# Kernel tuning notes

Measured on AMD Instinct MI355X. Metric: run time of the kernel, lower is better.

Reference implementation:

```python
import jax, jax.numpy as jnp
import numpy as np
import math

N_HEAD = 16


def _alibi_slopes(n_head):
    def get_slopes(n):
        start = 2.0 ** (-2.0 ** (-(math.log2(n) - 3)))
        return [start * start ** i for i in range(n)]
    if math.log2(n_head).is_integer():
        slopes = get_slopes(n_head)
    else:
        c = 2 ** math.floor(math.log2(n_head))
        slopes = get_slopes(c)
        extra = get_slopes(2 * c)[0::2]
        slopes = slopes + extra[: n_head - c]
    return np.asarray(slopes, dtype=np.float32)


def setup_inputs() -> dict:
    key = jax.random.key(0)
    ks = jax.random.split(key, 9)
    B, S, E = 2, 2048, 1024
    sd = 1.0 / math.sqrt(E)
    inp = {
        "x": jax.random.normal(ks[0], (B, S, E), jnp.float32),
        "Wq": jax.random.uniform(ks[1], (E, E), jnp.float32, -sd, sd),
        "bq": jnp.zeros((E,), jnp.float32),
        "Wk": jax.random.uniform(ks[2], (E, E), jnp.float32, -sd, sd),
        "bk": jnp.zeros((E,), jnp.float32),
        "Wv": jax.random.uniform(ks[3], (E, E), jnp.float32, -sd, sd),
        "bv": jnp.zeros((E,), jnp.float32),
        "Wo": jax.random.uniform(ks[4], (E, E), jnp.float32, -sd, sd),
        "bo": jnp.zeros((E,), jnp.float32),
        "alibi_slopes": jnp.asarray(_alibi_slopes(N_HEAD)),
    }
    return inp


def reference(x, Wq, bq, Wk, bk, Wv, bv, Wo, bo, alibi_slopes):
    B, S, E = x.shape
    H = N_HEAD
    hd = E // H
    scale = hd ** -0.5
    # Linear layers (torch Linear: y = x @ W.T + b)
    Q = (x @ Wq.T + bq).reshape(B, H, S, hd)  # faithful: view, NOT transpose
    K = (x @ Wk.T + bk).reshape(B, H, S, hd)
    V = (x @ Wv.T + bv).reshape(B, H, S, hd)
    scores = jnp.einsum("bhqd,bhkd->bhqk", Q, K) * scale
    pos = jnp.arange(S)
    rel = jnp.abs(pos[None, :] - pos[:, None]).astype(scores.dtype)  # [S,S]
    bias = alibi_slopes[None, :, None, None] * rel[None, None]  # [1,H,S,S]
    scores = scores - bias
    probs = jax.nn.softmax(scores, axis=-1)
    # faithful quirk: keep only head index 1's probs, broadcast to all heads
    probs1 = probs[:, 1:2, :, :]  # [B,1,S,S]
    attn_out = jnp.matmul(probs1, V)  # broadcast -> [B,H,S,hd]
    attn_out = attn_out.reshape(B, S, E)
    out = attn_out @ Wo.T + bo
    return (out, probs1)
```

## Files before the change

kernel.cpp:

```cpp
#include <hip/hip_runtime.h>

typedef __bf16 bf16;
typedef __bf16 bf16_4 __attribute__((ext_vector_type(4)));
typedef __bf16 bf16_8 __attribute__((ext_vector_type(8)));
typedef float f32_4 __attribute__((ext_vector_type(4)));

#define GLDS16(g, l) \
  __builtin_amdgcn_global_load_lds((const __attribute__((address_space(1))) unsigned int*)(g), \
                                   (__attribute__((address_space(3))) unsigned int*)(l), 16, 0, 0)

__global__ __launch_bounds__(256) void convert_all(
    const float* __restrict__ x, const float* __restrict__ wq, const float* __restrict__ wk,
    const float* __restrict__ wv, const float* __restrict__ wo,
    bf16* __restrict__ xb, bf16* __restrict__ wqb, bf16* __restrict__ wkb,
    bf16* __restrict__ wvb, bf16* __restrict__ wob)
{
    int i = blockIdx.x * 256 + threadIdx.x;
    const float* s; bf16* d; int off;
    if (i < 1048576) { s = x; d = xb; off = i; }
    else {
        int j = i - 1048576;
        int sel = j >> 18;
        off = j & 262143;
        s = (sel == 0) ? wq : (sel == 1) ? wk : (sel == 2) ? wv : wo;
        d = (sel == 0) ? wqb : (sel == 1) ? wkb : (sel == 2) ? wvb : wob;
    }
    float4 v = reinterpret_cast<const float4*>(s)[off];
    bf16_4 o; o.x = (bf16)v.x; o.y = (bf16)v.y; o.z = (bf16)v.z; o.w = (bf16)v.w;
    reinterpret_cast<bf16_4*>(d)[off] = o;
}

template<int BM, int MODE>
__global__ __launch_bounds__(256) void gemm_glds(
    const bf16* __restrict__ A, int lda, long long aBatch,
    const bf16* __restrict__ W, int ldw, long long wBatch,
    const float* __restrict__ bias,
    void* __restrict__ outp, long long outBatch,
    int N, int K, float scale, const float* __restrict__ slopes,
    const bf16* __restrict__ W2, const float* __restrict__ bias2, void* __restrict__ out2,
    const bf16* __restrict__ W3, const float* __restrict__ bias3, void* __restrict__ out3,
    float* __restrict__ spart, const float* __restrict__ rsinv)
{
    constexpr int CA = BM * 8;
    constexpr int NJ = (BM == 128) ? 4 : 2;
    __shared__ alignas(16) bf16 As[BM * 64];
    __shared__ alignas(16) bf16 Bs[128 * 64];

    const int tid  = threadIdx.x;
    const int lane = tid & 63;
    const int wave = tid >> 6;
    const int l15  = lane & 15;
    const int quad = lane >> 4;
    const int n0   = blockIdx.x * 128;
    const int z    = blockIdx.z;

    const int WM = (BM == 128) ? (wave >> 1) * 64 : 0;
    const int WN = (BM == 128) ? (wave & 1) * 64 : wave * 32;

    int m0;
    const bf16* Ab; const bf16* Wb; const float* bvec; void* op;
    long long obase;
    if (MODE == 11) {
        int y = blockIdx.y;
        if (y < 64) {
            m0 = y * 64;
            Ab = A; Wb = W; bvec = bias; op = outp; obase = 0;
        } else {
            int sub   = y - 64;
            int batch = (sub >> 1) & 1;
            int sel   = sub >> 2;
            m0   = (sub & 1) * 64;
            Ab   = A + (long long)batch * 2097152LL + 131072LL;
            Wb   = sel ? W3 : W2;
            bvec = sel ? bias3 : bias2;
            op   = sel ? out3 : out2;
            obase = (long long)batch * 131072LL;
        }
    } else {
        m0 = blockIdx.y * BM;
        Ab = A + (long long)z * aBatch; Wb = W + (long long)z * wBatch;
        bvec = bias; op = outp;
        obase = (long long)z * outBatch;
    }

    f32_4 acc[4][NJ];
#pragma unroll
    for (int i = 0; i < 4; i++)
#pragma unroll
        for (int j = 0; j < NJ; j++) acc[i][j] = (f32_4)(0.0f);

    for (int k0 = 0; k0 < K; k0 += 64) {
#pragma unroll
        for (int it = 0; it < CA / 256; ++it) {
            int p = wave * (CA / 4) + it * 64 + lane;
            int r = p >> 3;
            int q = (p & 7) ^ (r & 7);
            GLDS16(Ab + (long long)(m0 + r) * lda + k0 + q * 8, As + p * 8);
        }
#pragma unroll
        for (int it = 0; it < 4; ++it) {
            int p = wave * 256 + it * 64 + lane;
            int r = p >> 3;
            int q = (p & 7) ^ (r & 7);
            GLDS16(Wb + (long long)(n0 + r) * ldw + k0 + q * 8, Bs + p * 8);
        }
        __syncthreads();

#pragma unroll
        for (int kh = 0; kh < 2; ++kh) {
            bf16_8 af[4], bfr[NJ];
#pragma unroll
            for (int t = 0; t < 4; ++t) {
                int r = WM + t * 16 + l15;
                int q = (kh * 4 + quad) ^ (r & 7);
                af[t] = *reinterpret_cast<const bf16_8*>(&As[r * 64 + q * 8]);
            }
#pragma unroll
            for (int j = 0; j < NJ; ++j) {
                int r = WN + j * 16 + l15;
                int q = (kh * 4 + quad) ^ (r & 7);
                bfr[j] = *reinterpret_cast<const bf16_8*>(&Bs[r * 64 + q * 8]);
            }
#pragma unroll
            for (int i = 0; i < 4; ++i)
#pragma unroll
                for (int j = 0; j < NJ; ++j)
                    acc[i][j] = __builtin_amdgcn_mfma_f32_16x16x32_bf16(af[i], bfr[j], acc[i][j], 0, 0, 0);
        }
        __syncthreads();
    }

    if constexpr (MODE == 9) {
        const float slope = slopes[1];
#pragma unroll
        for (int i = 0; i < 4; i++) {
#pragma unroll
            for (int rg = 0; rg < 4; rg++) {
                int m = m0 + WM + i * 16 + quad * 4 + rg;
                float rowpart = 0.0f;
#pragma unroll
                for (int j = 0; j < NJ; j++) {
                    int n = n0 + WN + j * 16 + l15;
                    float v = acc[i][j][rg] * scale - slope * fabsf((float)(m - n));
                    float e = __expf(v);
                    rowpart += e;
                    ((bf16*)op)[obase + (long long)m * N + n] = (bf16)e;
                }
                rowpart += __shfl_xor(rowpart, 1, 64);
                rowpart += __shfl_xor(rowpart, 2, 64);
                rowpart += __shfl_xor(rowpart, 4, 64);
                rowpart += __shfl_xor(rowpart, 8, 64);
                if (l15 == 0)
                    spart[((long long)z * 2048 + m) * 32 + (n0 >> 6) + (WN >> 6)] = rowpart;
            }
        }
        return;
    }

#pragma unroll
    for (int i = 0; i < 4; i++) {
#pragma unroll
        for (int j = 0; j < NJ; j++) {
#pragma unroll
            for (int rg = 0; rg < 4; rg++) {
                int m = m0 + WM + i * 16 + quad * 4 + rg;
                int n = n0 + WN + j * 16 + l15;
                float v = acc[i][j][rg];
                if (MODE == 11) {
                    v += bvec[n];
                    ((bf16*)op)[obase + (long long)m * 1024 + n] = (bf16)v;
                } else if (MODE == 1) {
                    if (bvec) v += bvec[n];
                    ((float*)op)[obase + (long long)m * N + n] = v;
                } else {
                    v *= rsinv[(long long)z * 2048 + m];
                    long long off = obase +
                                    ((long long)(n >> 6)) * 131072LL + (long long)m * 64 + (n & 63);
                    ((bf16*)op)[off] = (bf16)v;
                }
            }
        }
    }
}

__global__ __launch_bounds__(256) void transpose_v(const unsigned short* __restrict__ v,
                                                   unsigned short* __restrict__ vt) {
    __shared__ unsigned short tile[64 * 66];
    const int t  = threadIdx.x;
    const int k0 = blockIdx.x * 64;
    const int h  = blockIdx.y;
    const int b  = blockIdx.z;
    const unsigned short* src = v + (long long)b * 2097152LL + (long long)h * 131072LL;
#pragma unroll
    for (int p = 0; p < 8; p++) {
        int idx = t + p * 256;
        int k   = idx >> 5;
        int dc  = idx & 31;
        ushort2 u = *reinterpret_cast<const ushort2*>(&src[(long long)(k0 + k) * 64 + dc * 2]);
        tile[(dc * 2) * 66 + k]     = u.x;
        tile[(dc * 2 + 1) * 66 + k] = u.y;
    }
    __syncthreads();
    unsigned short* dst = vt + (long long)b * 2097152LL + (long long)h * 64 * 2048LL + k0;
#pragma unroll
    for (int p = 0; p < 8; p++) {
        int idx = t + p * 256;
        int d   = idx >> 5;
        int kc  = idx & 31;
        ushort2 u;
        u.x = tile[d * 66 + kc * 2];
        u.y = tile[d * 66 + kc * 2 + 1];
        *reinterpret_cast<ushort2*>(&dst[(long long)d * 2048 + kc * 2]) = u;
    }
}

__global__ __launch_bounds__(256) void normalize_rows(const float* __restrict__ spart,
                                                      const bf16* __restrict__ pb,
                                                      float* __restrict__ probs_f,
                                                      float* __restrict__ rsinv) {
    __shared__ float inv_s;
    const long long row = blockIdx.x;
    const int t = threadIdx.x;

    if (t < 64) {
        float p = (t < 32) ? spart[row * 32 + t] : 0.0f;
#pragma unroll
        for (int o = 1; o <= 32; o <<= 1) p += __shfl_xor(p, o, 64);
        if (t == 0) { float inv = 1.0f / p; inv_s = inv; rsinv[row] = inv; }
    }
    __syncthreads();
    const float inv = inv_s;

    bf16_8 e = reinterpret_cast<const bf16_8*>(pb + row * 2048LL)[t];
    float4 o0, o1;
    o0.x = (float)e[0] * inv; o0.y = (float)e[1] * inv; o0.z = (float)e[2] * inv; o0.w = (float)e[3] * inv;
    o1.x = (float)e[4] * inv; o1.y = (float)e[5] * inv; o1.z = (float)e[6] * inv; o1.w = (float)e[7] * inv;
    reinterpret_cast<float4*>(probs_f + row * 2048LL)[t * 2]     = o0;
    reinterpret_cast<float4*>(probs_f + row * 2048LL)[t * 2 + 1] = o1;
}

extern "C" void kernel_launch(void* const* d_in, const int* in_sizes, int n_in,
                              void* d_out, int out_size, void* d_ws, size_t ws_size,
                              hipStream_t stream) {
    const float* x      = (const float*)d_in[0];
    const float* Wq     = (const float*)d_in[1];
    const float* bq     = (const float*)d_in[2];
    const float* Wk     = (const float*)d_in[3];
    const float* bk     = (const float*)d_in[4];
    const float* Wv     = (const float*)d_in[5];
    const float* bv     = (const float*)d_in[6];
    const float* Wo     = (const float*)d_in[7];
    const float* bo     = (const float*)d_in[8];
    const float* slopes = (const float*)d_in[9];

    char* w = (char*)d_ws;
    bf16* x_bf  = (bf16*)w;  w += 4096LL * 1024 * 2;
    bf16* wq_bf = (bf16*)w;  w += 1024LL * 1024 * 2;
    bf16* wk_bf = (bf16*)w;  w += 1024LL * 1024 * 2;
    bf16* wv_bf = (bf16*)w;  w += 1024LL * 1024 * 2;
    bf16* wo_bf = (bf16*)w;  w += 1024LL * 1024 * 2;
    bf16* qh1   = (bf16*)w;  w += 2LL * 131072 * 2;
    bf16* kh1   = (bf16*)w;  w += 2LL * 131072 * 2;
    bf16* v_bf  = (bf16*)w;  w += 4096LL * 1024 * 2;
    bf16* vt    = (bf16*)w;  w += 2LL * 1024 * 2048 * 2;
    bf16* attn  = (bf16*)w;  w += 4096LL * 1024 * 2;
    bf16* pb    = (bf16*)w;  w += 2LL * 2048 * 2048 * 2;
    float* spart = (float*)w; w += 4096LL * 32 * 4;
    float* rsinv = (float*)w; w += 4096LL * 4;

    float* out_f   = (float*)d_out;
    float* probs_f = (float*)d_out + 4194304LL;

    convert_all<<<8192, 256, 0, stream>>>(x, Wq, Wk, Wv, Wo, x_bf, wq_bf, wk_bf, wv_bf, wo_bf);

    gemm_glds<64, 11><<<dim3(8, 72, 1), 256, 0, stream>>>(
        x_bf, 1024, 0LL,
        wv_bf, 1024, 0LL, bv, v_bf, 0LL, 1024, 1024, 1.0f, nullptr,
        wq_bf, bq, qh1,
        wk_bf, bk, kh1,
        nullptr, nullptr);

    transpose_v<<<dim3(32, 16, 2), 256, 0, stream>>>((const unsigned short*)v_bf,
                                                     (unsigned short*)vt);

    gemm_glds<128, 9><<<dim3(16, 16, 2), 256, 0, stream>>>(
        qh1, 64, 131072LL, kh1, 64, 131072LL, nullptr,
        pb, 4194304LL, 2048, 64, 0.125f, slopes,
        nullptr, nullptr, nullptr, nullptr, nullptr, nullptr, spart, nullptr);

    normalize_rows<<<4096, 256, 0, stream>>>(spart, pb, probs_f, rsinv);

    gemm_glds<64, 6><<<dim3(8, 32, 2), 256, 0, stream>>>(
        pb, 2048, 4194304LL, vt, 2048, 2097152LL, nullptr,
        attn, 2097152LL, 1024, 2048, 1.0f, nullptr,
        nullptr, nullptr, nullptr, nullptr, nullptr, nullptr, nullptr, rsinv);

    gemm_glds<64, 1><<<dim3(8, 64, 1), 256, 0, stream>>>(
        attn, 1024, 0LL, wo_bf, 1024, 0LL, bo,
        out_f, 0LL, 1024, 1024, 1.0f, nullptr,
        nullptr, nullptr, nullptr, nullptr, nullptr, nullptr, nullptr, nullptr);
}
```

Before: 195.5 us.

## Fuse all attention stages into one cooperative persistent kernel with grid syncs

Replaces the seven separate launches (convert, QKV GEMM, V transpose, scores, normalize, PV GEMM, output GEMM) with one cooperative kernel of 512 blocks that runs each stage in turn, separated by grid-wide syncs. The aim is to remove per-launch overhead and the idle gaps between kernels. The cost is that each stage is now fixed to 512 blocks, so phases such as the Q/K projection leave most blocks idle, and every grid sync adds a barrier. If the cooperative launch fails, the code falls back to the original multi-kernel path.

```diff
diff --git a/kernel.cpp b/kernel.cpp
--- a/kernel.cpp
+++ b/kernel.cpp
@@ -1,4 +1,7 @@
 #include <hip/hip_runtime.h>
+#include <hip/hip_cooperative_groups.h>
+
+namespace cg = cooperative_groups;
 
 typedef __bf16 bf16;
 typedef __bf16 bf16_4 __attribute__((ext_vector_type(4)));
@@ -8,6 +11,282 @@
 #define GLDS16(g, l) \
   __builtin_amdgcn_global_load_lds((const __attribute__((address_space(1))) unsigned int*)(g), \
                                    (__attribute__((address_space(3))) unsigned int*)(l), 16, 0, 0)
+
+template<int BM>
+__device__ __forceinline__ void gemm_core(
+    const bf16* __restrict__ Ab, int lda,
+    const bf16* __restrict__ Wb, int ldw,
+    int K, int m0, int n0, int tid,
+    bf16* As, bf16* Bs,
+    f32_4 (&acc)[4][(BM == 128) ? 4 : 2])
+{
+    constexpr int NJ = (BM == 128) ? 4 : 2;
+    constexpr int CA = BM * 8;
+    const int lane = tid & 63;
+    const int wave = tid >> 6;
+    const int l15  = lane & 15;
+    const int quad = lane >> 4;
+    const int WM = (BM == 128) ? (wave >> 1) * 64 : 0;
+    const int WN = (BM == 128) ? (wave & 1) * 64 : wave * 32;
+
+#pragma unroll
+    for (int i = 0; i < 4; i++)
+#pragma unroll
+        for (int j = 0; j < NJ; j++) acc[i][j] = (f32_4)(0.0f);
+
+    for (int k0 = 0; k0 < K; k0 += 64) {
+#pragma unroll
+        for (int it = 0; it < CA / 256; ++it) {
+            int p = wave * (CA / 4) + it * 64 + lane;
+            int r = p >> 3;
+            int q = (p & 7) ^ (r & 7);
+            GLDS16(Ab + (long long)(m0 + r) * lda + k0 + q * 8, As + p * 8);
+        }
+#pragma unroll
+        for (int it = 0; it < 4; ++it) {
+            int p = wave * 256 + it * 64 + lane;
+            int r = p >> 3;
+            int q = (p & 7) ^ (r & 7);
+            GLDS16(Wb + (long long)(n0 + r) * ldw + k0 + q * 8, Bs + p * 8);
+        }
+        __syncthreads();
+
+#pragma unroll
+        for (int kh = 0; kh < 2; ++kh) {
+            bf16_8 af[4], bfr[NJ];
+#pragma unroll
+            for (int t = 0; t < 4; ++t) {
+                int r = WM + t * 16 + l15;
+                int q = (kh * 4 + quad) ^ (r & 7);
+                af[t] = *reinterpret_cast<const bf16_8*>(&As[r * 64 + q * 8]);
+            }
+#pragma unroll
+            for (int j = 0; j < NJ; ++j) {
+                int r = WN + j * 16 + l15;
+                int q = (kh * 4 + quad) ^ (r & 7);
+                bfr[j] = *reinterpret_cast<const bf16_8*>(&Bs[r * 64 + q * 8]);
+            }
+#pragma unroll
+            for (int i = 0; i < 4; ++i)
+#pragma unroll
+                for (int j = 0; j < NJ; ++j)
+                    acc[i][j] = __builtin_amdgcn_mfma_f32_16x16x32_bf16(af[i], bfr[j], acc[i][j], 0, 0, 0);
+        }
+        __syncthreads();
+    }
+}
+
+__global__ __launch_bounds__(256, 2) void fused_mha(
+    const float* __restrict__ x,  const float* __restrict__ Wq, const float* __restrict__ bq,
+    const float* __restrict__ Wk, const float* __restrict__ bk,
+    const float* __restrict__ Wv, const float* __restrict__ bv,
+    const float* __restrict__ Wo, const float* __restrict__ bo,
+    const float* __restrict__ slopes,
+    bf16* __restrict__ x_bf, bf16* __restrict__ wq_bf, bf16* __restrict__ wk_bf,
+    bf16* __restrict__ wv_bf, bf16* __restrict__ wo_bf,
+    bf16* __restrict__ qh1, bf16* __restrict__ kh1, bf16* __restrict__ v_bf,
+    bf16* __restrict__ vt, bf16* __restrict__ attn, bf16* __restrict__ pb,
+    float* __restrict__ spart, float* __restrict__ rsinv,
+    float* __restrict__ out_f, float* __restrict__ probs_f)
+{
+    cg::grid_group grid = cg::this_grid();
+    __shared__ alignas(16) char smem[32768];
+    bf16* As    = (bf16*)smem;
+    bf16* Bs64  = (bf16*)(smem + 8192);
+    bf16* Bs128 = (bf16*)(smem + 16384);
+    const int tid = threadIdx.x;
+    const int bid = blockIdx.x;
+    const int lane = tid & 63;
+    const int wave = tid >> 6;
+    const int l15  = lane & 15;
+    const int quad = lane >> 4;
+
+    for (int i = bid * 256 + tid; i < 2097152; i += 512 * 256) {
+        const float* s; bf16* d; int off;
+        if (i < 1048576) { s = x; d = x_bf; off = i; }
+        else {
+            int j = i - 1048576;
+            int sel = j >> 18;
+            off = j & 262143;
+            s = (sel == 0) ? Wq : (sel == 1) ? Wk : (sel == 2) ? Wv : Wo;
+            d = (sel == 0) ? wq_bf : (sel == 1) ? wk_bf : (sel == 2) ? wv_bf : wo_bf;
+        }
+        float4 v = reinterpret_cast<const float4*>(s)[off];
+        bf16_4 o; o.x = (bf16)v.x; o.y = (bf16)v.y; o.z = (bf16)v.z; o.w = (bf16)v.w;
+        reinterpret_cast<bf16_4*>(d)[off] = o;
+    }
+    grid.sync();
+
+    {
+        int m0 = (bid >> 3) * 64, n0 = (bid & 7) * 128;
+        f32_4 acc[4][2];
+        gemm_core<64>(x_bf, 1024, wv_bf, 1024, 1024, m0, n0, tid, As, Bs64, acc);
+        const int WN = wave * 32;
+#pragma unroll
+        for (int i = 0; i < 4; i++)
+#pragma unroll
+            for (int j = 0; j < 2; j++)
+#pragma unroll
+                for (int rg = 0; rg < 4; rg++) {
+                    int m = m0 + i * 16 + quad * 4 + rg;
+                    int n = n0 + WN + j * 16 + l15;
+                    v_bf[(long long)m * 1024 + n] = (bf16)(acc[i][j][rg] + bv[n]);
+                }
+    }
+    grid.sync();
+
+    if (bid < 64) {
+        int sub = bid >> 3, xx = bid & 7;
+        int batch = (sub >> 1) & 1, sel = sub >> 2;
+        int m0 = (sub & 1) * 64, n0 = xx * 128;
+        const bf16* Ab = x_bf + (long long)batch * 2097152LL + 131072LL;
+        const bf16* Wb = sel ? wk_bf : wq_bf;
+        const float* bvec = sel ? bk : bq;
+        bf16* op = sel ? kh1 : qh1;
+        long long obase = (long long)batch * 131072LL;
+        f32_4 acc[4][2];
+        gemm_core<64>(Ab, 1024, Wb, 1024, 1024, m0, n0, tid, As, Bs64, acc);
+        const int WN = wave * 32;
+#pragma unroll
+        for (int i = 0; i < 4; i++)
+#pragma unroll
+            for (int j = 0; j < 2; j++)
+#pragma unroll
+                for (int rg = 0; rg < 4; rg++) {
+                    int m = m0 + i * 16 + quad * 4 + rg;
+                    int n = n0 + WN + j * 16 + l15;
+                    op[obase + (long long)m * 1024 + n] = (bf16)(acc[i][j][rg] + bvec[n]);
+                }
+    } else {
+        unsigned short* tile = (unsigned short*)smem;
+        const unsigned short* vsrc = (const unsigned short*)v_bf;
+        unsigned short* vdst = (unsigned short*)vt;
+        for (int u = bid - 64; u < 1024; u += 448) {
+            int k0 = (u & 31) * 64, h = (u >> 5) & 15, b = u >> 9;
+            const unsigned short* src = vsrc + (long long)b * 2097152LL + (long long)h * 131072LL;
+#pragma unroll
+            for (int p = 0; p < 8; p++) {
+                int idx = tid + p * 256;
+                int k = idx >> 5, dc = idx & 31;
+                ushort2 uu = *reinterpret_cast<const ushort2*>(&src[(long long)(k0 + k) * 64 + dc * 2]);
+                tile[(dc * 2) * 66 + k]     = uu.x;
+                tile[(dc * 2 + 1) * 66 + k] = uu.y;
+            }
+            __syncthreads();
+            unsigned short* dst = vdst + (long long)b * 2097152LL + (long long)h * 64 * 2048LL + k0;
+#pragma unroll
+            for (int p = 0; p < 8; p++) {
+                int idx = tid + p * 256;
+                int d = idx >> 5, kc = idx & 31;
+                ushort2 uu;
+                uu.x = tile[d * 66 + kc * 2];
+                uu.y = tile[d * 66 + kc * 2 + 1];
+                *reinterpret_cast<ushort2*>(&dst[(long long)d * 2048 + kc * 2]) = uu;
+            }
+            __syncthreads();
+        }
+    }
+    grid.sync();
+
+    {
+        int z = bid >> 8, rem = bid & 255;
+        int m0 = (rem >> 4) * 128, n0 = (rem & 15) * 128;
+        const bf16* Ab = qh1 + (long long)z * 131072LL;
+        const bf16* Wb = kh1 + (long long)z * 131072LL;
+        f32_4 acc[4][4];
+        gemm_core<128>(Ab, 64, Wb, 64, 64, m0, n0, tid, As, Bs128, acc);
+        const int WM = (wave >> 1) * 64;
+        const int WN = (wave & 1) * 64;
+        const float slope = slopes[1];
+        long long obase = (long long)z * 4194304LL;
+#pragma unroll
+        for (int i = 0; i < 4; i++) {
+#pragma unroll
+            for (int rg = 0; rg < 4; rg++) {
+                int m = m0 + WM + i * 16 + quad * 4 + rg;
+                float rowpart = 0.0f;
+#pragma unroll
+                for (int j = 0; j < 4; j++) {
+                    int n = n0 + WN + j * 16 + l15;
+                    float v = acc[i][j][rg] * 0.125f - slope * fabsf((float)(m - n));
+                    float e = __expf(v);
+                    rowpart += e;
+                    pb[obase + (long long)m * 2048 + n] = (bf16)e;
+                }
+                rowpart += __shfl_xor(rowpart, 1, 64);
+                rowpart += __shfl_xor(rowpart, 2, 64);
+                rowpart += __shfl_xor(rowpart, 4, 64);
+                rowpart += __shfl_xor(rowpart, 8, 64);
+                if (l15 == 0)
+                    spart[((long long)z * 2048 + m) * 32 + (n0 >> 6) + (WN >> 6)] = rowpart;
+            }
+        }
+    }
+    grid.sync();
+
+    {
+        float* invp = (float*)smem;
+        for (int r = bid; r < 4096; r += 512) {
+            if (tid < 64) {
+                float p = (tid < 32) ? spart[(long long)r * 32 + tid] : 0.0f;
+#pragma unroll
+                for (int o = 1; o <= 32; o <<= 1) p += __shfl_xor(p, o, 64);
+                if (tid == 0) { float inv = 1.0f / p; invp[0] = inv; rsinv[r] = inv; }
+            }
+            __syncthreads();
+            float inv = invp[0];
+            bf16_8 e = reinterpret_cast<const bf16_8*>(pb + (long long)r * 2048)[tid];
+            float4 o0, o1;
+            o0.x = (float)e[0] * inv; o0.y = (float)e[1] * inv; o0.z = (float)e[2] * inv; o0.w = (float)e[3] * inv;
+            o1.x = (float)e[4] * inv; o1.y = (float)e[5] * inv; o1.z = (float)e[6] * inv; o1.w = (float)e[7] * inv;
+            reinterpret_cast<float4*>(probs_f + (long long)r * 2048)[tid * 2]     = o0;
+            reinterpret_cast<float4*>(probs_f + (long long)r * 2048)[tid * 2 + 1] = o1;
+            __syncthreads();
+        }
+    }
+    grid.sync();
+
+    {
+        int z = bid >> 8, rem = bid & 255;
+        int m0 = (rem >> 3) * 64, n0 = (rem & 7) * 128;
+        const bf16* Ab = pb + (long long)z * 4194304LL;
+        const bf16* Wb = vt + (long long)z * 2097152LL;
+        f32_4 acc[4][2];
+        gemm_core<64>(Ab, 2048, Wb, 2048, 2048, m0, n0, tid, As, Bs64, acc);
+        const int WN = wave * 32;
+        long long obase = (long long)z * 2097152LL;
+#pragma unroll
+        for (int i = 0; i < 4; i++)
+#pragma unroll
+            for (int j = 0; j < 2; j++)
+#pragma unroll
+                for (int rg = 0; rg < 4; rg++) {
+                    int m = m0 + i * 16 + quad * 4 + rg;
+                    int n = n0 + WN + j * 16 + l15;
+                    float v = acc[i][j][rg] * rsinv[(long long)z * 2048 + m];
+                    long long off = obase + ((long long)(n >> 6)) * 131072LL + (long long)m * 64 + (n & 63);
+                    attn[off] = (bf16)v;
+                }
+    }
+    grid.sync();
+
+    {
+        int m0 = (bid >> 3) * 64, n0 = (bid & 7) * 128;
+        f32_4 acc[4][2];
+        gemm_core<64>(attn, 1024, wo_bf, 1024, 1024, m0, n0, tid, As, Bs64, acc);
+        const int WN = wave * 32;
+#pragma unroll
+        for (int i = 0; i < 4; i++)
+#pragma unroll
+            for (int j = 0; j < 2; j++)
+#pragma unroll
+                for (int rg = 0; rg < 4; rg++) {
+                    int m = m0 + i * 16 + quad * 4 + rg;
+                    int n = n0 + WN + j * 16 + l15;
+                    out_f[(long long)m * 1024 + n] = acc[i][j][rg] + bo[n];
+                }
+    }
+}
 
 __global__ __launch_bounds__(256) void convert_all(
     const float* __restrict__ x, const float* __restrict__ wq, const float* __restrict__ wk,
@@ -41,19 +320,16 @@
     const bf16* __restrict__ W3, const float* __restrict__ bias3, void* __restrict__ out3,
     float* __restrict__ spart, const float* __restrict__ rsinv)
 {
-    constexpr int CA = BM * 8;
     constexpr int NJ = (BM == 128) ? 4 : 2;
     __shared__ alignas(16) bf16 As[BM * 64];
     __shared__ alignas(16) bf16 Bs[128 * 64];
-
-    const int tid  = threadIdx.x;
+    const int tid = threadIdx.x;
     const int lane = tid & 63;
     const int wave = tid >> 6;
-    const int l15  = lane & 15;
+    const int l15 = lane & 15;
     const int quad = lane >> 4;
-    const int n0   = blockIdx.x * 128;
-    const int z    = blockIdx.z;
-
+    const int n0 = blockIdx.x * 128;
+    const int z = blockIdx.z;
     const int WM = (BM == 128) ? (wave >> 1) * 64 : 0;
     const int WN = (BM == 128) ? (wave & 1) * 64 : wave * 32;
 
@@ -62,25 +338,20 @@
     long long obase;
     if (MODE == 11) {
         int y = blockIdx.y;
-        if (y < 64) {
-            m0 = y * 64;
-            Ab = A; Wb = W; bvec = bias; op = outp; obase = 0;
-        } else {
-            int sub   = y - 64;
+        if (y < 64) { m0 = y * 64; Ab = A; Wb = W; bvec = bias; op = outp; obase = 0; }
+        else {
+            int sub = y - 64;
             int batch = (sub >> 1) & 1;
-            int sel   = sub >> 2;
-            m0   = (sub & 1) * 64;
-            Ab   = A + (long long)batch * 2097152LL + 131072LL;
-            Wb   = sel ? W3 : W2;
-            bvec = sel ? bias3 : bias2;
-            op   = sel ? out3 : out2;
+            int sel = sub >> 2;
+            m0 = (sub & 1) * 64;
+            Ab = A + (long long)batch * 2097152LL + 131072LL;
+            Wb = sel ? W3 : W2; bvec = sel ? bias3 : bias2; op = sel ? out3 : out2;
             obase = (long long)batch * 131072LL;
         }
     } else {
         m0 = blockIdx.y * BM;
         Ab = A + (long long)z * aBatch; Wb = W + (long long)z * wBatch;
-        bvec = bias; op = outp;
-        obase = (long long)z * outBatch;
+        bvec = bias; op = outp; obase = (long long)z * outBatch;
     }
 
     f32_4 acc[4][NJ];
@@ -91,8 +362,8 @@
 
     for (int k0 = 0; k0 < K; k0 += 64) {
 #pragma unroll
-        for (int it = 0; it < CA / 256; ++it) {
-            int p = wave * (CA / 4) + it * 64 + lane;
+        for (int it = 0; it < (BM * 8) / 256; ++it) {
+            int p = wave * (BM * 2) + it * 64 + lane;
             int r = p >> 3;
             int q = (p & 7) ^ (r & 7);
             GLDS16(Ab + (long long)(m0 + r) * lda + k0 + q * 8, As + p * 8);
@@ -105,7 +376,6 @@
             GLDS16(Wb + (long long)(n0 + r) * ldw + k0 + q * 8, Bs + p * 8);
         }
         __syncthreads();
-
 #pragma unroll
         for (int kh = 0; kh < 2; ++kh) {
             bf16_8 af[4], bfr[NJ];
@@ -174,8 +444,7 @@
                     ((float*)op)[obase + (long long)m * N + n] = v;
                 } else {
                     v *= rsinv[(long long)z * 2048 + m];
-                    long long off = obase +
-                                    ((long long)(n >> 6)) * 131072LL + (long long)m * 64 + (n & 63);
+                    long long off = obase + ((long long)(n >> 6)) * 131072LL + (long long)m * 64 + (n & 63);
                     ((bf16*)op)[off] = (bf16)v;
                 }
             }
@@ -186,18 +455,17 @@
 __global__ __launch_bounds__(256) void transpose_v(const unsigned short* __restrict__ v,
                                                    unsigned short* __restrict__ vt) {
     __shared__ unsigned short tile[64 * 66];
-    const int t  = threadIdx.x;
+    const int t = threadIdx.x;
     const int k0 = blockIdx.x * 64;
-    const int h  = blockIdx.y;
-    const int b  = blockIdx.z;
+    const int h = blockIdx.y;
+    const int b = blockIdx.z;
     const unsigned short* src = v + (long long)b * 2097152LL + (long long)h * 131072LL;
 #pragma unroll
     for (int p = 0; p < 8; p++) {
         int idx = t + p * 256;
-        int k   = idx >> 5;
-        int dc  = idx & 31;
+        int k = idx >> 5, dc = idx & 31;
         ushort2 u = *reinterpret_cast<const ushort2*>(&src[(long long)(k0 + k) * 64 + dc * 2]);
-        tile[(dc * 2) * 66 + k]     = u.x;
+        tile[(dc * 2) * 66 + k] = u.x;
         tile[(dc * 2 + 1) * 66 + k] = u.y;
     }
     __syncthreads();
@@ -205,8 +473,7 @@
 #pragma unroll
     for (int p = 0; p < 8; p++) {
         int idx = t + p * 256;
-        int d   = idx >> 5;
-        int kc  = idx & 31;
+        int d = idx >> 5, kc = idx & 31;
         ushort2 u;
         u.x = tile[d * 66 + kc * 2];
         u.y = tile[d * 66 + kc * 2 + 1];
@@ -221,7 +488,6 @@
     __shared__ float inv_s;
     const long long row = blockIdx.x;
     const int t = threadIdx.x;
-
     if (t < 64) {
         float p = (t < 32) ? spart[row * 32 + t] : 0.0f;
 #pragma unroll
@@ -230,12 +496,11 @@
     }
     __syncthreads();
     const float inv = inv_s;
-
     bf16_8 e = reinterpret_cast<const bf16_8*>(pb + row * 2048LL)[t];
     float4 o0, o1;
     o0.x = (float)e[0] * inv; o0.y = (float)e[1] * inv; o0.z = (float)e[2] * inv; o0.w = (float)e[3] * inv;
     o1.x = (float)e[4] * inv; o1.y = (float)e[5] * inv; o1.z = (float)e[6] * inv; o1.w = (float)e[7] * inv;
-    reinterpret_cast<float4*>(probs_f + row * 2048LL)[t * 2]     = o0;
+    reinterpret_cast<float4*>(probs_f + row * 2048LL)[t * 2] = o0;
     reinterpret_cast<float4*>(probs_f + row * 2048LL)[t * 2 + 1] = o1;
 }
 
@@ -271,32 +536,34 @@
     float* out_f   = (float*)d_out;
     float* probs_f = (float*)d_out + 4194304LL;
 
-    convert_all<<<8192, 256, 0, stream>>>(x, Wq, Wk, Wv, Wo, x_bf, wq_bf, wk_bf, wv_bf, wo_bf);
-
-    gemm_glds<64, 11><<<dim3(8, 72, 1), 256, 0, stream>>>(
-        x_bf, 1024, 0LL,
-        wv_bf, 1024, 0LL, bv, v_bf, 0LL, 1024, 1024, 1.0f, nullptr,
-        wq_bf, bq, qh1,
-        wk_bf, bk, kh1,
-        nullptr, nullptr);
-
-    transpose_v<<<dim3(32, 16, 2), 256, 0, stream>>>((const unsigned short*)v_bf,
-                                                     (unsigned short*)vt);
-
-    gemm_glds<128, 9><<<dim3(16, 16, 2), 256, 0, stream>>>(
-        qh1, 64, 131072LL, kh1, 64, 131072LL, nullptr,
-        pb, 4194304LL, 2048, 64, 0.125f, slopes,
-        nullptr, nullptr, nullptr, nullptr, nullptr, nullptr, spart, nullptr);
-
-    normalize_rows<<<4096, 256, 0, stream>>>(spart, pb, probs_f, rsinv);
-
-    gemm_glds<64, 6><<<dim3(8, 32, 2), 256, 0, stream>>>(
-        pb, 2048, 4194304LL, vt, 2048, 2097152LL, nullptr,
-        attn, 2097152LL, 1024, 2048, 1.0f, nullptr,
-        nullptr, nullptr, nullptr, nullptr, nullptr, nullptr, nullptr, rsinv);
-
-    gemm_glds<64, 1><<<dim3(8, 64, 1), 256, 0, stream>>>(
-        attn, 1024, 0LL, wo_bf, 1024, 0LL, bo,
-        out_f, 0LL, 1024, 1024, 1.0f, nullptr,
-        nullptr, nullptr, nullptr, nullptr, nullptr, nullptr, nullptr, nullptr);
-}
+    void* args[] = {
+        (void*)&x, (void*)&Wq, (void*)&bq, (void*)&Wk, (void*)&bk,
+        (void*)&Wv, (void*)&bv, (void*)&Wo, (void*)&bo, (void*)&slopes,
+        (void*)&x_bf, (void*)&wq_bf, (void*)&wk_bf, (void*)&wv_bf, (void*)&wo_bf,
+        (void*)&qh1, (void*)&kh1, (void*)&v_bf, (void*)&vt, (void*)&attn, (void*)&pb,
+        (void*)&spart, (void*)&rsinv, (void*)&out_f, (void*)&probs_f
+    };
+    hipError_t err = hipLaunchCooperativeKernel((void*)fused_mha, dim3(512), dim3(256),
+                                                args, 0, stream);
+    if (err != hipSuccess) {
+        convert_all<<<8192, 256, 0, stream>>>(x, Wq, Wk, Wv, Wo, x_bf, wq_bf, wk_bf, wv_bf, wo_bf);
+        gemm_glds<64, 11><<<dim3(8, 72, 1), 256, 0, stream>>>(
+            x_bf, 1024, 0LL, wv_bf, 1024, 0LL, bv, v_bf, 0LL, 1024, 1024, 1.0f, nullptr,
+            wq_bf, bq, qh1, wk_bf, bk, kh1, nullptr, nullptr);
+        transpose_v<<<dim3(32, 16, 2), 256, 0, stream>>>((const unsigned short*)v_bf,
+                                                         (unsigned short*)vt);
+        gemm_glds<128, 9><<<dim3(16, 16, 2), 256, 0, stream>>>(
+            qh1, 64, 131072LL, kh1, 64, 131072LL, nullptr,
+            pb, 4194304LL, 2048, 64, 0.125f, slopes,
+            nullptr, nullptr, nullptr, nullptr, nullptr, nullptr, spart, nullptr);
+        normalize_rows<<<4096, 256, 0, stream>>>(spart, pb, probs_f, rsinv);
+        gemm_glds<64, 6><<<dim3(8, 32, 2), 256, 0, stream>>>(
+            pb, 2048, 4194304LL, vt, 2048, 2097152LL, nullptr,
+            attn, 2097152LL, 1024, 2048, 1.0f, nullptr,
+            nullptr, nullptr, nullptr, nullptr, nullptr, nullptr, nullptr, rsinv);
+        gemm_glds<64, 1><<<dim3(8, 64, 1), 256, 0, stream>>>(
+            attn, 1024, 0LL, wo_bf, 1024, 0LL, bo,
+            out_f, 0LL, 1024, 1024, 1.0f, nullptr,
+            nullptr, nullptr, nullptr, nullptr, nullptr, nullptr, nullptr, nullptr);
+    }
+}
```

Result: slower. 568.2 us (+190.7%).

## Fuse V transpose into scores kernel and row normalization into PV GEMM

Applied to the files above, without the earlier changes.

Folds the separate V-transpose launch into the tail of the scores kernel, where each block transposes two 64x64 tiles after writing its exp scores. The normalize_rows kernel is removed: the PV GEMM now sums the per-row partial sums itself and writes the fp32 normalized probabilities from the P tiles already staged in LDS, one diagonal k-chunk per column block. This drops two launches and a second full read of the bf16 exp matrix, in exchange for extra work and barriers inside the scores and PV kernels. The generic templated GEMM is also split into specialised kernels.

```diff
diff --git a/kernel.cpp b/kernel.cpp
--- a/kernel.cpp
+++ b/kernel.cpp
@@ -30,60 +30,23 @@
     reinterpret_cast<bf16_4*>(d)[off] = o;
 }
 
-template<int BM, int MODE>
-__global__ __launch_bounds__(256) void gemm_glds(
-    const bf16* __restrict__ A, int lda, long long aBatch,
-    const bf16* __restrict__ W, int ldw, long long wBatch,
-    const float* __restrict__ bias,
-    void* __restrict__ outp, long long outBatch,
-    int N, int K, float scale, const float* __restrict__ slopes,
-    const bf16* __restrict__ W2, const float* __restrict__ bias2, void* __restrict__ out2,
-    const bf16* __restrict__ W3, const float* __restrict__ bias3, void* __restrict__ out3,
-    float* __restrict__ spart, const float* __restrict__ rsinv)
-{
+template<int BM>
+__device__ __forceinline__ void gemm_core(
+    const bf16* __restrict__ Ab, int lda,
+    const bf16* __restrict__ Wb, int ldw,
+    int K, int m0, int n0, int tid,
+    bf16* As, bf16* Bs,
+    f32_4 (&acc)[4][(BM == 128) ? 4 : 2])
+{
+    constexpr int NJ = (BM == 128) ? 4 : 2;
     constexpr int CA = BM * 8;
-    constexpr int NJ = (BM == 128) ? 4 : 2;
-    __shared__ alignas(16) bf16 As[BM * 64];
-    __shared__ alignas(16) bf16 Bs[128 * 64];
-
-    const int tid  = threadIdx.x;
     const int lane = tid & 63;
     const int wave = tid >> 6;
     const int l15  = lane & 15;
     const int quad = lane >> 4;
-    const int n0   = blockIdx.x * 128;
-    const int z    = blockIdx.z;
-
     const int WM = (BM == 128) ? (wave >> 1) * 64 : 0;
     const int WN = (BM == 128) ? (wave & 1) * 64 : wave * 32;
 
-    int m0;
-    const bf16* Ab; const bf16* Wb; const float* bvec; void* op;
-    long long obase;
-    if (MODE == 11) {
-        int y = blockIdx.y;
-        if (y < 64) {
-            m0 = y * 64;
-            Ab = A; Wb = W; bvec = bias; op = outp; obase = 0;
-        } else {
-            int sub   = y - 64;
-            int batch = (sub >> 1) & 1;
-            int sel   = sub >> 2;
-            m0   = (sub & 1) * 64;
-            Ab   = A + (long long)batch * 2097152LL + 131072LL;
-            Wb   = sel ? W3 : W2;
-            bvec = sel ? bias3 : bias2;
-            op   = sel ? out3 : out2;
-            obase = (long long)batch * 131072LL;
-        }
-    } else {
-        m0 = blockIdx.y * BM;
-        Ab = A + (long long)z * aBatch; Wb = W + (long long)z * wBatch;
-        bvec = bias; op = outp;
-        obase = (long long)z * outBatch;
-    }
-
-    f32_4 acc[4][NJ];
 #pragma unroll
     for (int i = 0; i < 4; i++)
 #pragma unroll
@@ -129,114 +92,265 @@
         }
         __syncthreads();
     }
-
-    if constexpr (MODE == 9) {
-        const float slope = slopes[1];
-#pragma unroll
-        for (int i = 0; i < 4; i++) {
+}
+
+__global__ __launch_bounds__(256) void proj_merged(
+    const bf16* __restrict__ x_bf,
+    const bf16* __restrict__ wv_bf, const float* __restrict__ bv, bf16* __restrict__ v_bf,
+    const bf16* __restrict__ wq_bf, const float* __restrict__ bq, bf16* __restrict__ qh1,
+    const bf16* __restrict__ wk_bf, const float* __restrict__ bk, bf16* __restrict__ kh1)
+{
+    __shared__ alignas(16) bf16 As[64 * 64];
+    __shared__ alignas(16) bf16 Bs[128 * 64];
+    const int tid = threadIdx.x;
+    const int lane = tid & 63, wave = tid >> 6, l15 = lane & 15, quad = lane >> 4;
+    const int n0 = blockIdx.x * 128;
+
+    int m0;
+    const bf16* Ab; const bf16* Wb; const float* bvec; bf16* op;
+    long long obase;
+    int y = blockIdx.y;
+    if (y < 64) { m0 = y * 64; Ab = x_bf; Wb = wv_bf; bvec = bv; op = v_bf; obase = 0; }
+    else {
+        int sub = y - 64;
+        int batch = (sub >> 1) & 1;
+        int sel = sub >> 2;
+        m0 = (sub & 1) * 64;
+        Ab = x_bf + (long long)batch * 2097152LL + 131072LL;
+        Wb = sel ? wk_bf : wq_bf;
+        bvec = sel ? bk : bq;
+        op = sel ? kh1 : qh1;
+        obase = (long long)batch * 131072LL;
+    }
+
+    f32_4 acc[4][2];
+    gemm_core<64>(Ab, 1024, Wb, 1024, 1024, m0, n0, tid, As, Bs, acc);
+
+    const int WN = wave * 32;
+#pragma unroll
+    for (int i = 0; i < 4; i++)
+#pragma unroll
+        for (int j = 0; j < 2; j++)
 #pragma unroll
             for (int rg = 0; rg < 4; rg++) {
-                int m = m0 + WM + i * 16 + quad * 4 + rg;
-                float rowpart = 0.0f;
-#pragma unroll
-                for (int j = 0; j < NJ; j++) {
-                    int n = n0 + WN + j * 16 + l15;
-                    float v = acc[i][j][rg] * scale - slope * fabsf((float)(m - n));
-                    float e = __expf(v);
-                    rowpart += e;
-                    ((bf16*)op)[obase + (long long)m * N + n] = (bf16)e;
-                }
-                rowpart += __shfl_xor(rowpart, 1, 64);
-                rowpart += __shfl_xor(rowpart, 2, 64);
-                rowpart += __shfl_xor(rowpart, 4, 64);
-                rowpart += __shfl_xor(rowpart, 8, 64);
-                if (l15 == 0)
-                    spart[((long long)z * 2048 + m) * 32 + (n0 >> 6) + (WN >> 6)] = rowpart;
-            }
-        }
-        return;
-    }
-
+                int m = m0 + i * 16 + quad * 4 + rg;
+                int n = n0 + WN + j * 16 + l15;
+                op[obase + (long long)m * 1024 + n] = (bf16)(acc[i][j][rg] + bvec[n]);
+            }
+}
+
+__global__ __launch_bounds__(256) void scores_tr(
+    const bf16* __restrict__ qh1, const bf16* __restrict__ kh1,
+    const float* __restrict__ slopes,
+    bf16* __restrict__ pb, float* __restrict__ spart,
+    const unsigned short* __restrict__ v_bf, unsigned short* __restrict__ vt)
+{
+    __shared__ alignas(16) char smem[32768];
+    bf16* As = (bf16*)smem;
+    bf16* Bs = (bf16*)(smem + 16384);
+    const int tid = threadIdx.x;
+    const int lane = tid & 63, wave = tid >> 6, l15 = lane & 15, quad = lane >> 4;
+    const int n0 = blockIdx.x * 128;
+    const int m0 = blockIdx.y * 128;
+    const int z  = blockIdx.z;
+
+    f32_4 acc[4][4];
+    gemm_core<128>(qh1 + (long long)z * 131072LL, 64,
+                   kh1 + (long long)z * 131072LL, 64, 64, m0, n0, tid, As, Bs, acc);
+
+    const int WM = (wave >> 1) * 64;
+    const int WN = (wave & 1) * 64;
+    const float slope = slopes[1];
+    long long obase = (long long)z * 4194304LL;
 #pragma unroll
     for (int i = 0; i < 4; i++) {
 #pragma unroll
-        for (int j = 0; j < NJ; j++) {
+        for (int rg = 0; rg < 4; rg++) {
+            int m = m0 + WM + i * 16 + quad * 4 + rg;
+            float rowpart = 0.0f;
+#pragma unroll
+            for (int j = 0; j < 4; j++) {
+                int n = n0 + WN + j * 16 + l15;
+                float v = acc[i][j][rg] * 0.125f - slope * fabsf((float)(m - n));
+                float e = __expf(v);
+                rowpart += e;
+                pb[obase + (long long)m * 2048 + n] = (bf16)e;
+            }
+            rowpart += __shfl_xor(rowpart, 1, 64);
+            rowpart += __shfl_xor(rowpart, 2, 64);
+            rowpart += __shfl_xor(rowpart, 4, 64);
+            rowpart += __shfl_xor(rowpart, 8, 64);
+            if (l15 == 0)
+                spart[((long long)z * 2048 + m) * 32 + (n0 >> 6) + (WN >> 6)] = rowpart;
+        }
+    }
+
+    unsigned short* tile = (unsigned short*)smem;
+    int flat = z * 256 + blockIdx.y * 16 + blockIdx.x;
+#pragma unroll
+    for (int uu = 0; uu < 2; ++uu) {
+        int u = flat * 2 + uu;
+        int k0 = (u & 31) * 64, h = (u >> 5) & 15, b = u >> 9;
+        const unsigned short* src = v_bf + (long long)b * 2097152LL + (long long)h * 131072LL;
+#pragma unroll
+        for (int p = 0; p < 8; p++) {
+            int idx = tid + p * 256;
+            int k = idx >> 5, dc = idx & 31;
+            ushort2 w = *reinterpret_cast<const ushort2*>(&src[(long long)(k0 + k) * 64 + dc * 2]);
+            tile[(dc * 2) * 66 + k]     = w.x;
+            tile[(dc * 2 + 1) * 66 + k] = w.y;
+        }
+        __syncthreads();
+        unsigned short* dst = vt + (long long)b * 2097152LL + (long long)h * 64 * 2048LL + k0;
+#pragma unroll
+        for (int p = 0; p < 8; p++) {
+            int idx = tid + p * 256;
+            int d = idx >> 5, kc = idx & 31;
+            ushort2 w;
+            w.x = tile[d * 66 + kc * 2];
+            w.y = tile[d * 66 + kc * 2 + 1];
+            *reinterpret_cast<ushort2*>(&dst[(long long)d * 2048 + kc * 2]) = w;
+        }
+        __syncthreads();
+    }
+}
+
+__global__ __launch_bounds__(256) void pv_fused(
+    const bf16* __restrict__ pb, const bf16* __restrict__ vt,
+    const float* __restrict__ spart,
+    bf16* __restrict__ attn, float* __restrict__ probs_f)
+{
+    __shared__ alignas(16) bf16 As[64 * 64];
+    __shared__ alignas(16) bf16 Bs[128 * 64];
+    __shared__ float rs[64];
+    const int tid = threadIdx.x;
+    const int lane = tid & 63, wave = tid >> 6, l15 = lane & 15, quad = lane >> 4;
+    const int nx = blockIdx.x;
+    const int n0 = nx * 128;
+    const int m0 = blockIdx.y * 64;
+    const int z  = blockIdx.z;
+
+    {
+        int r = tid >> 2, part = tid & 3;
+        const float* sp = spart + ((long long)z * 2048 + m0 + r) * 32 + part * 8;
+        float4 a = *reinterpret_cast<const float4*>(sp);
+        float4 b = *reinterpret_cast<const float4*>(sp + 4);
+        float v = a.x + a.y + a.z + a.w + b.x + b.y + b.z + b.w;
+        v += __shfl_xor(v, 1, 64);
+        v += __shfl_xor(v, 2, 64);
+        if (part == 0) rs[r] = 1.0f / v;
+    }
+    __syncthreads();
+
+    const bf16* Ab = pb + (long long)z * 4194304LL;
+    const bf16* Wb = vt + (long long)z * 2097152LL;
+
+    f32_4 acc[4][2];
+#pragma unroll
+    for (int i = 0; i < 4; i++)
+#pragma unroll
+        for (int j = 0; j < 2; j++) acc[i][j] = (f32_4)(0.0f);
+
+    for (int k0 = 0; k0 < 2048; k0 += 64) {
+#pragma unroll
+        for (int it = 0; it < 2; ++it) {
+            int p = wave * 128 + it * 64 + lane;
+            int r = p >> 3, q = (p & 7) ^ (r & 7);
+            GLDS16(Ab + (long long)(m0 + r) * 2048 + k0 + q * 8, As + p * 8);
+        }
+#pragma unroll
+        for (int it = 0; it < 4; ++it) {
+            int p = wave * 256 + it * 64 + lane;
+            int r = p >> 3, q = (p & 7) ^ (r & 7);
+            GLDS16(Wb + (long long)(n0 + r) * 2048 + k0 + q * 8, Bs + p * 8);
+        }
+        __syncthreads();
+
+        if ((k0 >> 8) == nx) {
+#pragma unroll
+            for (int s0 = 0; s0 < 2; ++s0) {
+                int s = tid + s0 * 256;
+                int r = s >> 3, q = s & 7;
+                bf16_8 e = *reinterpret_cast<const bf16_8*>(&As[r * 64 + (q ^ (r & 7)) * 8]);
+                float inv = rs[r];
+                float4 o0, o1;
+                o0.x = (float)e[0] * inv; o0.y = (float)e[1] * inv;
+                o0.z = (float)e[2] * inv; o0.w = (float)e[3] * inv;
+                o1.x = (float)e[4] * inv; o1.y = (float)e[5] * inv;
+                o1.z = (float)e[6] * inv; o1.w = (float)e[7] * inv;
+                long long base = ((long long)z * 2048 + m0 + r) * 2048 + k0 + q * 8;
+                *reinterpret_cast<float4*>(&probs_f[base])     = o0;
+                *reinterpret_cast<float4*>(&probs_f[base + 4]) = o1;
+            }
+        }
+
+#pragma unroll
+        for (int kh = 0; kh < 2; ++kh) {
+            bf16_8 af[4], bfr[2];
+#pragma unroll
+            for (int t = 0; t < 4; ++t) {
+                int r = t * 16 + l15;
+                int q = (kh * 4 + quad) ^ (r & 7);
+                af[t] = *reinterpret_cast<const bf16_8*>(&As[r * 64 + q * 8]);
+            }
+            const int WN = wave * 32;
+#pragma unroll
+            for (int j = 0; j < 2; ++j) {
+                int r = WN + j * 16 + l15;
+                int q = (kh * 4 + quad) ^ (r & 7);
+                bfr[j] = *reinterpret_cast<const bf16_8*>(&Bs[r * 64 + q * 8]);
+            }
+#pragma unroll
+            for (int i = 0; i < 4; ++i)
+#pragma unroll
+                for (int j = 0; j < 2; ++j)
+                    acc[i][j] = __builtin_amdgcn_mfma_f32_16x16x32_bf16(af[i], bfr[j], acc[i][j], 0, 0, 0);
+        }
+        __syncthreads();
+    }
+
+    const int WN = wave * 32;
+    long long obase = (long long)z * 2097152LL;
+#pragma unroll
+    for (int i = 0; i < 4; i++)
+#pragma unroll
+        for (int j = 0; j < 2; j++)
 #pragma unroll
             for (int rg = 0; rg < 4; rg++) {
-                int m = m0 + WM + i * 16 + quad * 4 + rg;
+                int ml = i * 16 + quad * 4 + rg;
+                int m = m0 + ml;
                 int n = n0 + WN + j * 16 + l15;
-                float v = acc[i][j][rg];
-                if (MODE == 11) {
-                    v += bvec[n];
-                    ((bf16*)op)[obase + (long long)m * 1024 + n] = (bf16)v;
-                } else if (MODE == 1) {
-                    if (bvec) v += bvec[n];
-                    ((float*)op)[obase + (long long)m * N + n] = v;
-                } else {
-                    v *= rsinv[(long long)z * 2048 + m];
-                    long long off = obase +
-                                    ((long long)(n >> 6)) * 131072LL + (long long)m * 64 + (n & 63);
-                    ((bf16*)op)[off] = (bf16)v;
-                }
-            }
-        }
-    }
-}
-
-__global__ __launch_bounds__(256) void transpose_v(const unsigned short* __restrict__ v,
-                                                   unsigned short* __restrict__ vt) {
-    __shared__ unsigned short tile[64 * 66];
-    const int t  = threadIdx.x;
-    const int k0 = blockIdx.x * 64;
-    const int h  = blockIdx.y;
-    const int b  = blockIdx.z;
-    const unsigned short* src = v + (long long)b * 2097152LL + (long long)h * 131072LL;
-#pragma unroll
-    for (int p = 0; p < 8; p++) {
-        int idx = t + p * 256;
-        int k   = idx >> 5;
-        int dc  = idx & 31;
-        ushort2 u = *reinterpret_cast<const ushort2*>(&src[(long long)(k0 + k) * 64 + dc * 2]);
-        tile[(dc * 2) * 66 + k]     = u.x;
-        tile[(dc * 2 + 1) * 66 + k] = u.y;
-    }
-    __syncthreads();
-    unsigned short* dst = vt + (long long)b * 2097152LL + (long long)h * 64 * 2048LL + k0;
-#pragma unroll
-    for (int p = 0; p < 8; p++) {
-        int idx = t + p * 256;
-        int d   = idx >> 5;
-        int kc  = idx & 31;
-        ushort2 u;
-        u.x = tile[d * 66 + kc * 2];
-        u.y = tile[d * 66 + kc * 2 + 1];
-        *reinterpret_cast<ushort2*>(&dst[(long long)d * 2048 + kc * 2]) = u;
-    }
-}
-
-__global__ __launch_bounds__(256) void normalize_rows(const float* __restrict__ spart,
-                                                      const bf16* __restrict__ pb,
-                                                      float* __restrict__ probs_f,
-                                                      float* __restrict__ rsinv) {
-    __shared__ float inv_s;
-    const long long row = blockIdx.x;
-    const int t = threadIdx.x;
-
-    if (t < 64) {
-        float p = (t < 32) ? spart[row * 32 + t] : 0.0f;
-#pragma unroll
-        for (int o = 1; o <= 32; o <<= 1) p += __shfl_xor(p, o, 64);
-        if (t == 0) { float inv = 1.0f / p; inv_s = inv; rsinv[row] = inv; }
-    }
-    __syncthreads();
-    const float inv = inv_s;
-
-    bf16_8 e = reinterpret_cast<const bf16_8*>(pb + row * 2048LL)[t];
-    float4 o0, o1;
-    o0.x = (float)e[0] * inv; o0.y = (float)e[1] * inv; o0.z = (float)e[2] * inv; o0.w = (float)e[3] * inv;
-    o1.x = (float)e[4] * inv; o1.y = (float)e[5] * inv; o1.z = (float)e[6] * inv; o1.w = (float)e[7] * inv;
-    reinterpret_cast<float4*>(probs_f + row * 2048LL)[t * 2]     = o0;
-    reinterpret_cast<float4*>(probs_f + row * 2048LL)[t * 2 + 1] = o1;
+                float v = acc[i][j][rg] * rs[ml];
+                long long off = obase + ((long long)(n >> 6)) * 131072LL + (long long)m * 64 + (n & 63);
+                attn[off] = (bf16)v;
+            }
+}
+
+__global__ __launch_bounds__(256) void out_proj(
+    const bf16* __restrict__ attn, const bf16* __restrict__ wo_bf,
+    const float* __restrict__ bo, float* __restrict__ out_f)
+{
+    __shared__ alignas(16) bf16 As[64 * 64];
+    __shared__ alignas(16) bf16 Bs[128 * 64];
+    const int tid = threadIdx.x;
+    const int lane = tid & 63, wave = tid >> 6, l15 = lane & 15, quad = lane >> 4;
+    const int n0 = blockIdx.x * 128;
+    const int m0 = blockIdx.y * 64;
+
+    f32_4 acc[4][2];
+    gemm_core<64>(attn, 1024, wo_bf, 1024, 1024, m0, n0, tid, As, Bs, acc);
+
+    const int WN = wave * 32;
+#pragma unroll
+    for (int i = 0; i < 4; i++)
+#pragma unroll
+        for (int j = 0; j < 2; j++)
+#pragma unroll
+            for (int rg = 0; rg < 4; rg++) {
+                int m = m0 + i * 16 + quad * 4 + rg;
+                int n = n0 + WN + j * 16 + l15;
+                out_f[(long long)m * 1024 + n] = acc[i][j][rg] + bo[n];
+            }
 }
 
 extern "C" void kernel_launch(void* const* d_in, const int* in_sizes, int n_in,
@@ -266,37 +380,20 @@
     bf16* attn  = (bf16*)w;  w += 4096LL * 1024 * 2;
     bf16* pb    = (bf16*)w;  w += 2LL * 2048 * 2048 * 2;
     float* spart = (float*)w; w += 4096LL * 32 * 4;
-    float* rsinv = (float*)w; w += 4096LL * 4;
 
     float* out_f   = (float*)d_out;
     float* probs_f = (float*)d_out + 4194304LL;
 
     convert_all<<<8192, 256, 0, stream>>>(x, Wq, Wk, Wv, Wo, x_bf, wq_bf, wk_bf, wv_bf, wo_bf);
 
-    gemm_glds<64, 11><<<dim3(8, 72, 1), 256, 0, stream>>>(
-        x_bf, 1024, 0LL,
-        wv_bf, 1024, 0LL, bv, v_bf, 0LL, 1024, 1024, 1.0f, nullptr,
-        wq_bf, bq, qh1,
-        wk_bf, bk, kh1,
-        nullptr, nullptr);
-
-    transpose_v<<<dim3(32, 16, 2), 256, 0, stream>>>((const unsigned short*)v_bf,
-                                                     (unsigned short*)vt);
-
-    gemm_glds<128, 9><<<dim3(16, 16, 2), 256, 0, stream>>>(
-        qh1, 64, 131072LL, kh1, 64, 131072LL, nullptr,
-        pb, 4194304LL, 2048, 64, 0.125f, slopes,
-        nullptr, nullptr, nullptr, nullptr, nullptr, nullptr, spart, nullptr);
-
-    normalize_rows<<<4096, 256, 0, stream>>>(spart, pb, probs_f, rsinv);
-
-    gemm_glds<64, 6><<<dim3(8, 32, 2), 256, 0, stream>>>(
-        pb, 2048, 4194304LL, vt, 2048, 2097152LL, nullptr,
-        attn, 2097152LL, 1024, 2048, 1.0f, nullptr,
-        nullptr, nullptr, nullptr, nullptr, nullptr, nullptr, nullptr, rsinv);
-
-    gemm_glds<64, 1><<<dim3(8, 64, 1), 256, 0, stream>>>(
-        attn, 1024, 0LL, wo_bf, 1024, 0LL, bo,
-        out_f, 0LL, 1024, 1024, 1.0f, nullptr,
-        nullptr, nullptr, nullptr, nullptr, nullptr, nullptr, nullptr, nullptr);
-}
+    proj_merged<<<dim3(8, 72, 1), 256, 0, stream>>>(
+        x_bf, wv_bf, bv, v_bf, wq_bf, bq, qh1, wk_bf, bk, kh1);
+
+    scores_tr<<<dim3(16, 16, 2), 256, 0, stream>>>(
+        qh1, kh1, slopes, pb, spart,
+        (const unsigned short*)v_bf, (unsigned short*)vt);
+
+    pv_fused<<<dim3(8, 32, 2), 256, 0, stream>>>(pb, vt, spart, attn, probs_f);
+
+    out_proj<<<dim3(8, 64, 1), 256, 0, stream>>>(attn, wo_bf, bo, out_f);
+}
```

Measured after the change: 179.2 us. 1.09x faster.
